# Performance work log

Measured on AMD Instinct MI355X. Metric: run time of the kernel, lower is better.

## Reference

```python
import jax, jax.numpy as jnp
import numpy as np

NUM_EMBEDDINGS = 512
EMBEDDING_DIM = 64
BETA = 0.25


def setup_inputs() -> dict:
    key = jax.random.key(0)
    k1, k2 = jax.random.split(key)
    latent_z = jax.random.normal(k1, (32, EMBEDDING_DIM, 64, 64), dtype=jnp.float32)
    # nn.Embedding init: uniform(-1/K, 1/K)
    scale = 1.0 / NUM_EMBEDDINGS
    embedding = jax.random.uniform(k2, (NUM_EMBEDDINGS, EMBEDDING_DIM), dtype=jnp.float32,
                                   minval=-scale, maxval=scale)
    return {"latent_z": latent_z, "embedding": embedding}


def reference(latent_z, embedding):
    # [B, C, H, W] -> [B, H, W, C]
    z = jnp.transpose(latent_z, (0, 2, 3, 1))
    B, H, W, D = z.shape
    flat_z = z.reshape(-1, D)  # [N, D]

    # squared L2 distances via expansion: ||z||^2 + ||e||^2 - 2 z.e
    dist = (jnp.sum(flat_z ** 2, axis=1, keepdims=True)
            + jnp.sum(embedding ** 2, axis=1)
            - 2.0 * flat_z @ embedding.T)  # [N, K]

    idx = jnp.argmin(dist, axis=1)  # [N]
    encodings = jax.nn.one_hot(idx, NUM_EMBEDDINGS, dtype=flat_z.dtype)  # [N, K]

    # gather codes (same math as one_hot @ embedding)
    quantized = embedding[idx].reshape(B, H, W, D)

    quant_loss = (jnp.mean((jax.lax.stop_gradient(quantized) - z) ** 2)
                  + BETA * jnp.mean((quantized - jax.lax.stop_gradient(z)) ** 2))

    # straight-through estimator
    quantized_st = z + jax.lax.stop_gradient(quantized - z)

    mean_enc = jnp.mean(encodings, axis=0)
    perplexity = jnp.exp(-jnp.sum(mean_enc * jnp.log(mean_enc + 1e-10)))

    quantized_out = jnp.transpose(quantized_st, (0, 3, 1, 2))  # back to [B, C, H, W]
    return quant_loss, quantized_out, perplexity, encodings, idx[:, None]
```

## Files before the change

### kernel.cpp

```cpp
#include <hip/hip_runtime.h>
#include <math.h>

#define NPIX   131072
#define KCODES 512
#define DIM    64
#define HW     4096
#define CHW    262144

#define O_Q    1ll
#define O_PERP 8388609ll
#define O_ENC  8388610ll
#define O_IDX  75497474ll


__device__ __forceinline__ float np_sumsq64(const float (&x)[64]) {
#pragma clang fp contract(off)
  float r0 = x[0]*x[0], r1 = x[1]*x[1], r2 = x[2]*x[2], r3 = x[3]*x[3];
  float r4 = x[4]*x[4], r5 = x[5]*x[5], r6 = x[6]*x[6], r7 = x[7]*x[7];
#pragma unroll
  for (int i = 8; i < 64; i += 8) {
    r0 += x[i+0]*x[i+0];
    r1 += x[i+1]*x[i+1];
    r2 += x[i+2]*x[i+2];
    r3 += x[i+3]*x[i+3];
    r4 += x[i+4]*x[i+4];
    r5 += x[i+5]*x[i+5];
    r6 += x[i+6]*x[i+6];
    r7 += x[i+7]*x[i+7];
  }
  return ((r0+r1)+(r2+r3))+((r4+r5)+(r6+r7));
}

__global__ void vq_prep(const float* __restrict__ emb, float* __restrict__ ws) {
  const int t = threadIdx.x;
  if (t == 0) ws[0] = 0.0f;
  ((unsigned*)ws)[1 + t] = 0u;
  float x[64];
  const float* e = emb + t * DIM;
#pragma unroll
  for (int d = 0; d < 64; ++d) x[d] = e[d];
  ws[513 + t] = np_sumsq64(x);
}

__global__ __launch_bounds__(512, 4)
void vq_main(
    const float* __restrict__ z, const float* __restrict__ emb,
    float* __restrict__ out, float* __restrict__ ws)
{
  __shared__ float ET_s[16 * 256];
  __shared__ float z_l[64 * 128];
  __shared__ float esq_l[512];
  __shared__ float zsq_l[128];
  __shared__ int   ridx_l[128];
  __shared__ float wsum[8];

  const int t   = threadIdx.x;
  const int ci  = t & 31;
  const int pi  = t >> 5;
  const int blk = blockIdx.x;
  const int n0  = blk * 128;
  const int b   = n0 >> 12;
  const int hw0 = n0 & 4095;
  const float* zg = z + (size_t)b * CHW + hw0;

  esq_l[t] = ws[513 + t];

  {
    const int i     = t & 31;
    const int dbase = t >> 5;
#pragma unroll
    for (int r = 0; r < 4; ++r) {
      const int d = dbase + 16 * r;
      *(float4*)&z_l[d * 128 + 4 * i] = *(const float4*)(zg + (size_t)d * HW + 4 * i);
    }
  }

  const int ec = t & 255;
  const int eh = t >> 8;
  float4 p0, p1;
  {
    const float* er = emb + (size_t)ec * 64 + 8 * eh;
    p0 = *(const float4*)(er + 0);
    p1 = *(const float4*)(er + 4);
  }

  __syncthreads();

  if (t < 128) {
    float x[64];
#pragma unroll
    for (int d = 0; d < 64; ++d) x[d] = z_l[d * 128 + t];
    zsq_l[t] = np_sumsq64(x);
  }

  float bd[8];
  int   bk[8];
#pragma unroll
  for (int j = 0; j < 8; ++j) { bd[j] = INFINITY; bk[j] = 0; }

  float2* encb = (float2*)(out + O_ENC) + (size_t)n0 * 256;
  const float2 zz = make_float2(0.0f, 0.0f);

  for (int H = 0; H < 2; ++H) {
    float acc[8][8];
#pragma unroll
    for (int j = 0; j < 8; ++j)
#pragma unroll
      for (int c = 0; c < 8; ++c) acc[j][c] = 0.0f;

    for (int s = 0; s < 4; ++s) {
      __syncthreads();
      {
        const float tmp[8] = {p0.x, p0.y, p0.z, p0.w, p1.x, p1.y, p1.z, p1.w};
#pragma unroll
        for (int dl = 0; dl < 8; ++dl) ET_s[(8 * eh + dl) * 256 + ec] = tmp[dl];
      }
      __syncthreads();

      if (!(H == 1 && s == 3)) {
        const int nH = (s < 3) ? H : 1;
        const int ns = (s < 3) ? (s + 1) : 0;
        const float* er = emb + (size_t)(256 * nH + ec) * 64 + 16 * ns + 8 * eh;
        p0 = *(const float4*)(er + 0);
        p1 = *(const float4*)(er + 4);
      }

      {
        const int batch = 4 * H + s;
#pragma unroll
        for (int u = 0; u < 8; ++u)
          encb[(size_t)batch * 4096 + u * 512 + t] = zz;
      }

#pragma unroll 2
      for (int dl = 0; dl < 16; ++dl) {
        const float* zp = &z_l[(16 * s + dl) * 128 + 8 * pi];
        const float4 za0 = *(const float4*)(zp + 0);
        const float4 za1 = *(const float4*)(zp + 4);
        const float* ep = &ET_s[dl * 256 + 4 * ci];
        const float4 e0 = *(const float4*)(ep + 0);
        const float4 e1 = *(const float4*)(ep + 128);
        const float zr[8] = {za0.x, za0.y, za0.z, za0.w,
                             za1.x, za1.y, za1.z, za1.w};
        const float er_[8] = {e0.x, e0.y, e0.z, e0.w,
                              e1.x, e1.y, e1.z, e1.w};
#pragma unroll
        for (int j = 0; j < 8; ++j)
#pragma unroll
          for (int c = 0; c < 8; ++c)
            acc[j][c] = fmaf(zr[j], er_[c], acc[j][c]);
      }
    }

#pragma unroll
    for (int q = 0; q < 2; ++q)
#pragma unroll
      for (int r = 0; r < 4; ++r) {
        const int k = 256 * H + 128 * q + 4 * ci + r;
        const float eq = esq_l[k];
#pragma unroll
        for (int j = 0; j < 8; ++j) {
          const float dist = (zsq_l[8 * pi + j] + eq) - 2.0f * acc[j][4 * q + r];
          if (dist < bd[j]) { bd[j] = dist; bk[j] = k; }
        }
      }
  }

#pragma unroll
  for (int m = 16; m >= 1; m >>= 1) {
#pragma unroll
    for (int j = 0; j < 8; ++j) {
      const float od = __shfl_xor(bd[j], m, 64);
      const int   ok = __shfl_xor(bk[j], m, 64);
      if (od < bd[j] || (od == bd[j] && ok < bk[j])) { bd[j] = od; bk[j] = ok; }
    }
  }
  if (ci == 0) {
#pragma unroll
    for (int j = 0; j < 8; ++j) ridx_l[8 * pi + j] = bk[j];
  }
  __syncthreads();

  if (t < 128) {
    const int k = ridx_l[t];
    out[O_IDX + n0 + t] = (float)k;
    atomicAdd((unsigned*)ws + 1 + k, 1u);
    out[O_ENC + (size_t)(n0 + t) * 512 + k] = 1.0f;
  }

  {
    const int px = t & 127;
    const int dq = t >> 7;
    const int k  = ridx_l[px];
    const float* e0 = emb + ((size_t)k << 6);
    float* q0 = out + O_Q + (size_t)b * CHW + hw0 + px;
    float lsum = 0.0f;
#pragma unroll
    for (int j = 0; j < 16; ++j) {
      const int d = dq * 16 + j;
      const float ev = e0[d];
      const float df = ev - z_l[d * 128 + px];
      lsum = fmaf(df, df, lsum);
      q0[(size_t)d * HW] = ev;
    }
#pragma unroll
    for (int off = 32; off > 0; off >>= 1) lsum += __shfl_down(lsum, off, 64);
    if ((t & 63) == 0) wsum[t >> 6] = lsum;
  }
  __syncthreads();
  if (t == 0)
    atomicAdd(ws, ((wsum[0] + wsum[1]) + (wsum[2] + wsum[3])) +
                  ((wsum[4] + wsum[5]) + (wsum[6] + wsum[7])));
}

__global__ void vq_fin(float* __restrict__ out, const float* __restrict__ ws) {
  __shared__ float red[8];
  const int t = threadIdx.x;
  const unsigned* counts = (const unsigned*)ws + 1;
  const float p = (float)counts[t] * (1.0f / 131072.0f);
  float h = p * logf(p + 1e-10f);
#pragma unroll
  for (int off = 32; off > 0; off >>= 1) h += __shfl_down(h, off, 64);
  if ((t & 63) == 0) red[t >> 6] = h;
  __syncthreads();
  if (t == 0) {
    float H = 0.0f;
#pragma unroll
    for (int w = 0; w < 8; ++w) H += red[w];
    out[O_PERP] = expf(-H);
    out[0] = 1.25f * ws[0] * (1.0f / 8388608.0f);
  }
}

extern "C" void kernel_launch(void* const* d_in, const int* in_sizes, int n_in,
                              void* d_out, int out_size, void* d_ws, size_t ws_size,
                              hipStream_t stream) {
  const float* z   = (const float*)d_in[0];
  const float* emb = (const float*)d_in[1];
  float* out = (float*)d_out;
  float* ws  = (float*)d_ws;

  vq_prep<<<1, 512, 0, stream>>>(emb, ws);
  vq_main<<<1024, 512, 0, stream>>>(z, emb, out, ws);
  vq_fin<<<1, 512, 0, stream>>>(out, ws);
}
```

Before: 426.0 us.

## Double-buffer codebook tiles and fold finalize into main kernel via last-block reduction

Codebook chunks now go into two alternating shared-memory buffers. This halves the block barriers per chunk and lets the next chunk's transpose-write overlap the current chunk's FMA loop. The separate finalize kernel is removed: the last block to finish, found with an atomic counter, computes perplexity and loss, which saves one kernel launch. In exchange the kernel uses more shared memory, which may reduce occupancy, and adds a threadfence plus an atomic at the end of every block.

```diff
diff --git a/kernel.cpp b/kernel.cpp
--- a/kernel.cpp
+++ b/kernel.cpp
@@ -6,6 +6,7 @@
 #define DIM    64
 #define HW     4096
 #define CHW    262144
+#define NBLK   1024
 
 #define O_Q    1ll
 #define O_PERP 8388609ll
@@ -33,13 +34,81 @@
 
 __global__ void vq_prep(const float* __restrict__ emb, float* __restrict__ ws) {
   const int t = threadIdx.x;
-  if (t == 0) ws[0] = 0.0f;
+  if (t == 0) { ws[0] = 0.0f; ((unsigned*)ws)[1025] = 0u; }
   ((unsigned*)ws)[1 + t] = 0u;
   float x[64];
   const float* e = emb + t * DIM;
 #pragma unroll
   for (int d = 0; d < 64; ++d) x[d] = e[d];
   ws[513 + t] = np_sumsq64(x);
+}
+
+
+__device__ __forceinline__ void et_prefetch(const float* __restrict__ emb,
+                                            int g, int ec, int eh,
+                                            float4& p0, float4& p1) {
+  const float* er = emb + (size_t)(256 * (g >> 2) + ec) * 64
+                        + 16 * (g & 3) + 8 * eh;
+  p0 = *(const float4*)(er + 0);
+  p1 = *(const float4*)(er + 4);
+}
+
+__device__ __forceinline__ void et_write(float* __restrict__ ETb,
+                                         const float4& p0, const float4& p1,
+                                         int eh, int ec) {
+  const float tmp[8] = {p0.x, p0.y, p0.z, p0.w, p1.x, p1.y, p1.z, p1.w};
+#pragma unroll
+  for (int dl = 0; dl < 8; ++dl) ETb[(8 * eh + dl) * 256 + ec] = tmp[dl];
+}
+
+__device__ __forceinline__ void enc_zero(float2* __restrict__ encb, int g, int t) {
+  const float2 zz = make_float2(0.0f, 0.0f);
+#pragma unroll
+  for (int u = 0; u < 8; ++u)
+    encb[(size_t)g * 4096 + u * 512 + t] = zz;
+}
+
+__device__ __forceinline__ void dl_loop(const float* __restrict__ ETb,
+                                        const float* __restrict__ zl,
+                                        int sdim, int pi, int ci,
+                                        float (&acc)[8][8]) {
+#pragma unroll 2
+  for (int dl = 0; dl < 16; ++dl) {
+    const float* zp = &zl[(sdim + dl) * 128 + 8 * pi];
+    const float4 za0 = *(const float4*)(zp + 0);
+    const float4 za1 = *(const float4*)(zp + 4);
+    const float* ep = &ETb[dl * 256 + 4 * ci];
+    const float4 e0 = *(const float4*)(ep + 0);
+    const float4 e1 = *(const float4*)(ep + 128);
+    const float zr[8] = {za0.x, za0.y, za0.z, za0.w,
+                         za1.x, za1.y, za1.z, za1.w};
+    const float er_[8] = {e0.x, e0.y, e0.z, e0.w,
+                          e1.x, e1.y, e1.z, e1.w};
+#pragma unroll
+    for (int j = 0; j < 8; ++j)
+#pragma unroll
+      for (int c = 0; c < 8; ++c)
+        acc[j][c] = fmaf(zr[j], er_[c], acc[j][c]);
+  }
+}
+
+__device__ __forceinline__ void dist_phase(int Hh, int ci, int pi,
+                                           const float (&acc)[8][8],
+                                           const float* __restrict__ esq_l,
+                                           const float* __restrict__ zsq_l,
+                                           float (&bd)[8], int (&bk)[8]) {
+#pragma unroll
+  for (int q = 0; q < 2; ++q)
+#pragma unroll
+    for (int r = 0; r < 4; ++r) {
+      const int k = 256 * Hh + 128 * q + 4 * ci + r;
+      const float eq = esq_l[k];
+#pragma unroll
+      for (int j = 0; j < 8; ++j) {
+        const float dist = (zsq_l[8 * pi + j] + eq) - 2.0f * acc[j][4 * q + r];
+        if (dist < bd[j]) { bd[j] = dist; bk[j] = k; }
+      }
+    }
 }
 
 __global__ __launch_bounds__(512, 4)
@@ -47,12 +116,13 @@
     const float* __restrict__ z, const float* __restrict__ emb,
     float* __restrict__ out, float* __restrict__ ws)
 {
-  __shared__ float ET_s[16 * 256];
+  __shared__ float ET_s[2][16 * 256];
   __shared__ float z_l[64 * 128];
   __shared__ float esq_l[512];
   __shared__ float zsq_l[128];
   __shared__ int   ridx_l[128];
   __shared__ float wsum[8];
+  __shared__ unsigned lflag;
 
   const int t   = threadIdx.x;
   const int ci  = t & 31;
@@ -78,11 +148,7 @@
   const int ec = t & 255;
   const int eh = t >> 8;
   float4 p0, p1;
-  {
-    const float* er = emb + (size_t)ec * 64 + 8 * eh;
-    p0 = *(const float4*)(er + 0);
-    p1 = *(const float4*)(er + 4);
-  }
+  et_prefetch(emb, 0, ec, eh, p0, p1);
 
   __syncthreads();
 
@@ -93,77 +159,51 @@
     zsq_l[t] = np_sumsq64(x);
   }
 
+  et_write(&ET_s[0][0], p0, p1, eh, ec);
+  et_prefetch(emb, 1, ec, eh, p0, p1);
+
+  __syncthreads();
+
   float bd[8];
   int   bk[8];
 #pragma unroll
   for (int j = 0; j < 8; ++j) { bd[j] = INFINITY; bk[j] = 0; }
+  float acc[8][8];
+#pragma unroll
+  for (int j = 0; j < 8; ++j)
+#pragma unroll
+    for (int c = 0; c < 8; ++c) acc[j][c] = 0.0f;
 
   float2* encb = (float2*)(out + O_ENC) + (size_t)n0 * 256;
-  const float2 zz = make_float2(0.0f, 0.0f);
-
-  for (int H = 0; H < 2; ++H) {
-    float acc[8][8];
-#pragma unroll
-    for (int j = 0; j < 8; ++j)
-#pragma unroll
-      for (int c = 0; c < 8; ++c) acc[j][c] = 0.0f;
-
-    for (int s = 0; s < 4; ++s) {
+
+  for (int gg = 0; gg < 4; ++gg) {
+    {
+      const int ge = 2 * gg;
+      et_write(&ET_s[1][0], p0, p1, eh, ec);
+      if (ge < 6) et_prefetch(emb, ge + 2, ec, eh, p0, p1);
+      enc_zero(encb, ge, t);
+      dl_loop(&ET_s[0][0], z_l, 16 * (ge & 3), pi, ci, acc);
       __syncthreads();
-      {
-        const float tmp[8] = {p0.x, p0.y, p0.z, p0.w, p1.x, p1.y, p1.z, p1.w};
-#pragma unroll
-        for (int dl = 0; dl < 8; ++dl) ET_s[(8 * eh + dl) * 256 + ec] = tmp[dl];
+    }
+    {
+      const int go = 2 * gg + 1;
+      if (go < 7) {
+        et_write(&ET_s[0][0], p0, p1, eh, ec);
+        et_prefetch(emb, go + 2, ec, eh, p0, p1);
+      }
+      enc_zero(encb, go, t);
+      dl_loop(&ET_s[1][0], z_l, 16 * (go & 3), pi, ci, acc);
+      if (gg & 1) {
+        dist_phase(gg >> 1, ci, pi, acc, esq_l, zsq_l, bd, bk);
+        if (gg == 1) {
+#pragma unroll
+          for (int j = 0; j < 8; ++j)
+#pragma unroll
+            for (int c = 0; c < 8; ++c) acc[j][c] = 0.0f;
+        }
       }
       __syncthreads();
-
-      if (!(H == 1 && s == 3)) {
-        const int nH = (s < 3) ? H : 1;
-        const int ns = (s < 3) ? (s + 1) : 0;
-        const float* er = emb + (size_t)(256 * nH + ec) * 64 + 16 * ns + 8 * eh;
-        p0 = *(const float4*)(er + 0);
-        p1 = *(const float4*)(er + 4);
-      }
-
-      {
-        const int batch = 4 * H + s;
-#pragma unroll
-        for (int u = 0; u < 8; ++u)
-          encb[(size_t)batch * 4096 + u * 512 + t] = zz;
-      }
-
-#pragma unroll 2
-      for (int dl = 0; dl < 16; ++dl) {
-        const float* zp = &z_l[(16 * s + dl) * 128 + 8 * pi];
-        const float4 za0 = *(const float4*)(zp + 0);
-        const float4 za1 = *(const float4*)(zp + 4);
-        const float* ep = &ET_s[dl * 256 + 4 * ci];
-        const float4 e0 = *(const float4*)(ep + 0);
-        const float4 e1 = *(const float4*)(ep + 128);
-        const float zr[8] = {za0.x, za0.y, za0.z, za0.w,
-                             za1.x, za1.y, za1.z, za1.w};
-        const float er_[8] = {e0.x, e0.y, e0.z, e0.w,
-                              e1.x, e1.y, e1.z, e1.w};
-#pragma unroll
-        for (int j = 0; j < 8; ++j)
-#pragma unroll
-          for (int c = 0; c < 8; ++c)
-            acc[j][c] = fmaf(zr[j], er_[c], acc[j][c]);
-      }
-    }
-
-#pragma unroll
-    for (int q = 0; q < 2; ++q)
-#pragma unroll
-      for (int r = 0; r < 4; ++r) {
-        const int k = 256 * H + 128 * q + 4 * ci + r;
-        const float eq = esq_l[k];
-#pragma unroll
-        for (int j = 0; j < 8; ++j) {
-          const float dist = (zsq_l[8 * pi + j] + eq) - 2.0f * acc[j][4 * q + r];
-          if (dist < bd[j]) { bd[j] = dist; bk[j] = k; }
-        }
-      }
+    }
   }
 
 #pragma unroll
@@ -211,24 +251,29 @@
   if (t == 0)
     atomicAdd(ws, ((wsum[0] + wsum[1]) + (wsum[2] + wsum[3])) +
                   ((wsum[4] + wsum[5]) + (wsum[6] + wsum[7])));
-}
-
-__global__ void vq_fin(float* __restrict__ out, const float* __restrict__ ws) {
-  __shared__ float red[8];
-  const int t = threadIdx.x;
-  const unsigned* counts = (const unsigned*)ws + 1;
-  const float p = (float)counts[t] * (1.0f / 131072.0f);
-  float h = p * logf(p + 1e-10f);
-#pragma unroll
-  for (int off = 32; off > 0; off >>= 1) h += __shfl_down(h, off, 64);
-  if ((t & 63) == 0) red[t >> 6] = h;
+
+  __threadfence();
   __syncthreads();
   if (t == 0) {
-    float H = 0.0f;
-#pragma unroll
-    for (int w = 0; w < 8; ++w) H += red[w];
-    out[O_PERP] = expf(-H);
-    out[0] = 1.25f * ws[0] * (1.0f / 8388608.0f);
+    const unsigned old = atomicAdd((unsigned*)ws + 1025, 1u);
+    lflag = (old == (unsigned)(NBLK - 1)) ? 1u : 0u;
+  }
+  __syncthreads();
+  if (lflag) {
+    const float p = (float)atomicAdd((unsigned*)ws + 1 + t, 0u)
+                    * (1.0f / 131072.0f);
+    float h = p * logf(p + 1e-10f);
+#pragma unroll
+    for (int off = 32; off > 0; off >>= 1) h += __shfl_down(h, off, 64);
+    if ((t & 63) == 0) wsum[t >> 6] = h;
+    __syncthreads();
+    if (t == 0) {
+      float Hs = 0.0f;
+#pragma unroll
+      for (int w = 0; w < 8; ++w) Hs += wsum[w];
+      out[O_PERP] = expf(-Hs);
+      out[0] = 1.25f * atomicAdd(ws, 0.0f) * (1.0f / 8388608.0f);
+    }
   }
 }
 
@@ -241,6 +286,5 @@
   float* ws  = (float*)d_ws;
 
   vq_prep<<<1, 512, 0, stream>>>(emb, ws);
-  vq_main<<<1024, 512, 0, stream>>>(z, emb, out, ws);
-  vq_fin<<<1, 512, 0, stream>>>(out, ws);
-}
+  vq_main<<<NBLK, 512, 0, stream>>>(z, emb, out, ws);
+}
```

After: 744.6 us. 74.8% more time.

## Retile VQ kernel to 64 pixels per block with all 512 codes at once

Applied to the files above, without the earlier changes.

Each block now handles 64 pixels against all 512 codes in one pass. The codebook is staged through a double-buffered transposed LDS tile with two codes interleaved per thread, and z is read directly from global memory (cache) instead of an LDS tile. The grid doubles to 2048 blocks, the one-hot zeroing and quantized writes use nontemporal 8-byte stores, and the z norm is computed as a cross-wave partial sum. This removes one sync per stage and halves the z footprint per block, at the cost of re-reading each codebook tile in twice as many blocks and loading z from global memory in the inner loop.

```diff
diff --git a/kernel.cpp b/kernel.cpp
--- a/kernel.cpp
+++ b/kernel.cpp
@@ -6,6 +6,7 @@
 #define DIM    64
 #define HW     4096
 #define CHW    262144
+#define NBLK   2048
 
 #define O_Q    1ll
 #define O_PERP 8388609ll
@@ -47,127 +48,130 @@
     const float* __restrict__ z, const float* __restrict__ emb,
     float* __restrict__ out, float* __restrict__ ws)
 {
-  __shared__ float ET_s[16 * 256];
-  __shared__ float z_l[64 * 128];
+  __shared__ float ET_s[2][16 * 512];
   __shared__ float esq_l[512];
-  __shared__ float zsq_l[128];
-  __shared__ int   ridx_l[128];
+  __shared__ float zsqp[512];
+  __shared__ float zsq_l[64];
+  __shared__ int   ridx_l[64];
   __shared__ float wsum[8];
 
-  const int t   = threadIdx.x;
-  const int ci  = t & 31;
-  const int pi  = t >> 5;
-  const int blk = blockIdx.x;
-  const int n0  = blk * 128;
-  const int b   = n0 >> 12;
-  const int hw0 = n0 & 4095;
+  const int t    = threadIdx.x;
+  const int lane = t & 63;
+  const int wv   = t >> 6;
+  const int blk  = blockIdx.x;
+  const int n0   = blk * 64;
+  const int b    = n0 >> 12;
+  const int hw0  = n0 & 4095;
   const float* zg = z + (size_t)b * CHW + hw0;
 
   esq_l[t] = ws[513 + t];
 
   {
-    const int i     = t & 31;
-    const int dbase = t >> 5;
-#pragma unroll
-    for (int r = 0; r < 4; ++r) {
-      const int d = dbase + 16 * r;
-      *(float4*)&z_l[d * 128 + 4 * i] = *(const float4*)(zg + (size_t)d * HW + 4 * i);
-    }
-  }
-
-  const int ec = t & 255;
-  const int eh = t >> 8;
-  float4 p0, p1;
-  {
-    const float* er = emb + (size_t)ec * 64 + 8 * eh;
-    p0 = *(const float4*)(er + 0);
-    p1 = *(const float4*)(er + 4);
-  }
-
-  __syncthreads();
-
-  if (t < 128) {
-    float x[64];
-#pragma unroll
-    for (int d = 0; d < 64; ++d) x[d] = z_l[d * 128 + t];
-    zsq_l[t] = np_sumsq64(x);
-  }
+#pragma clang fp contract(off)
+    float r = 0.0f;
+#pragma unroll
+    for (int m = 0; m < 8; ++m) {
+      const float x = zg[(size_t)(8 * m + wv) * HW + lane];
+      r += x * x;
+    }
+    zsqp[t] = r;
+  }
+
+  const int tc = t & 255;
+  const int th = t >> 8;
+  float pa[8], pb[8];
+  {
+    const float* ea = emb + (size_t)(2 * tc) * 64 + 8 * th;
+    const float* eb = ea + 64;
+#pragma unroll
+    for (int i = 0; i < 8; ++i) { pa[i] = ea[i]; pb[i] = eb[i]; }
+  }
+  {
+#pragma unroll
+    for (int i = 0; i < 8; ++i)
+      *(float2*)&ET_s[0][(8 * th + i) * 512 + 2 * tc] = make_float2(pa[i], pb[i]);
+  }
+  {
+    const float* ea = emb + (size_t)(2 * tc) * 64 + 16 + 8 * th;
+    const float* eb = ea + 64;
+#pragma unroll
+    for (int i = 0; i < 8; ++i) { pa[i] = ea[i]; pb[i] = eb[i]; }
+  }
+
+  __syncthreads();
 
   float bd[8];
   int   bk[8];
 #pragma unroll
   for (int j = 0; j < 8; ++j) { bd[j] = INFINITY; bk[j] = 0; }
-
-  float2* encb = (float2*)(out + O_ENC) + (size_t)n0 * 256;
-  const float2 zz = make_float2(0.0f, 0.0f);
-
-  for (int H = 0; H < 2; ++H) {
-    float acc[8][8];
-#pragma unroll
-    for (int j = 0; j < 8; ++j)
-#pragma unroll
-      for (int c = 0; c < 8; ++c) acc[j][c] = 0.0f;
-
-    for (int s = 0; s < 4; ++s) {
-      __syncthreads();
-      {
-        const float tmp[8] = {p0.x, p0.y, p0.z, p0.w, p1.x, p1.y, p1.z, p1.w};
-#pragma unroll
-        for (int dl = 0; dl < 8; ++dl) ET_s[(8 * eh + dl) * 256 + ec] = tmp[dl];
+  float acc[8][8];
+#pragma unroll
+  for (int j = 0; j < 8; ++j)
+#pragma unroll
+    for (int c = 0; c < 8; ++c) acc[j][c] = 0.0f;
+
+  double* encd = (double*)(out + O_ENC) + (size_t)n0 * 256;
+
+  for (int g = 0; g < 4; ++g) {
+    if (g < 3) {
+#pragma unroll
+      for (int i = 0; i < 8; ++i)
+        *(float2*)&ET_s[(g + 1) & 1][(8 * th + i) * 512 + 2 * tc] =
+            make_float2(pa[i], pb[i]);
+    }
+    if (g < 2) {
+      const float* ea = emb + (size_t)(2 * tc) * 64 + 16 * (g + 2) + 8 * th;
+      const float* eb = ea + 64;
+#pragma unroll
+      for (int i = 0; i < 8; ++i) { pa[i] = ea[i]; pb[i] = eb[i]; }
+    }
+#pragma unroll
+    for (int u = 0; u < 8; ++u)
+      __builtin_nontemporal_store(0.0, encd + (size_t)g * 4096 + u * 512 + t);
+    if (g == 0 && t < 64) {
+      zsq_l[t] = ((zsqp[t] + zsqp[64 + t]) + (zsqp[128 + t] + zsqp[192 + t])) +
+                 ((zsqp[256 + t] + zsqp[320 + t]) + (zsqp[384 + t] + zsqp[448 + t]));
+    }
+
+    const float* ETb = &ET_s[g & 1][0];
+#pragma unroll 2
+    for (int dl = 0; dl < 16; ++dl) {
+      const float* zrow = zg + (size_t)(16 * g + dl) * HW + 8 * wv;
+      const float4 za0 = *(const float4*)(zrow + 0);
+      const float4 za1 = *(const float4*)(zrow + 4);
+      const float* ep = &ETb[dl * 512 + 8 * lane];
+      const float4 e0 = *(const float4*)(ep + 0);
+      const float4 e1 = *(const float4*)(ep + 4);
+      const float zr[8] = {za0.x, za0.y, za0.z, za0.w,
+                           za1.x, za1.y, za1.z, za1.w};
+      const float er[8] = {e0.x, e0.y, e0.z, e0.w,
+                           e1.x, e1.y, e1.z, e1.w};
+#pragma unroll
+      for (int j = 0; j < 8; ++j)
+#pragma unroll
+        for (int c = 0; c < 8; ++c)
+          acc[j][c] = fmaf(zr[j], er[c], acc[j][c]);
+    }
+    __syncthreads();
+  }
+
+  {
+    const float4 q0 = *(const float4*)&esq_l[8 * lane];
+    const float4 q1 = *(const float4*)&esq_l[8 * lane + 4];
+    const float eqs[8] = {q0.x, q0.y, q0.z, q0.w, q1.x, q1.y, q1.z, q1.w};
+#pragma unroll
+    for (int r = 0; r < 8; ++r) {
+      const int k = 8 * lane + r;
+#pragma unroll
+      for (int j = 0; j < 8; ++j) {
+        const float dist = (zsq_l[8 * wv + j] + eqs[r]) - 2.0f * acc[j][r];
+        if (dist < bd[j]) { bd[j] = dist; bk[j] = k; }
       }
-      __syncthreads();
-
-      if (!(H == 1 && s == 3)) {
-        const int nH = (s < 3) ? H : 1;
-        const int ns = (s < 3) ? (s + 1) : 0;
-        const float* er = emb + (size_t)(256 * nH + ec) * 64 + 16 * ns + 8 * eh;
-        p0 = *(const float4*)(er + 0);
-        p1 = *(const float4*)(er + 4);
-      }
-
-      {
-        const int batch = 4 * H + s;
-#pragma unroll
-        for (int u = 0; u < 8; ++u)
-          encb[(size_t)batch * 4096 + u * 512 + t] = zz;
-      }
-
-#pragma unroll 2
-      for (int dl = 0; dl < 16; ++dl) {
-        const float* zp = &z_l[(16 * s + dl) * 128 + 8 * pi];
-        const float4 za0 = *(const float4*)(zp + 0);
-        const float4 za1 = *(const float4*)(zp + 4);
-        const float* ep = &ET_s[dl * 256 + 4 * ci];
-        const float4 e0 = *(const float4*)(ep + 0);
-        const float4 e1 = *(const float4*)(ep + 128);
-        const float zr[8] = {za0.x, za0.y, za0.z, za0.w,
-                             za1.x, za1.y, za1.z, za1.w};
-        const float er_[8] = {e0.x, e0.y, e0.z, e0.w,
-                              e1.x, e1.y, e1.z, e1.w};
-#pragma unroll
-        for (int j = 0; j < 8; ++j)
-#pragma unroll
-          for (int c = 0; c < 8; ++c)
-            acc[j][c] = fmaf(zr[j], er_[c], acc[j][c]);
-      }
-    }
-
-#pragma unroll
-    for (int q = 0; q < 2; ++q)
-#pragma unroll
-      for (int r = 0; r < 4; ++r) {
-        const int k = 256 * H + 128 * q + 4 * ci + r;
-        const float eq = esq_l[k];
-#pragma unroll
-        for (int j = 0; j < 8; ++j) {
-          const float dist = (zsq_l[8 * pi + j] + eq) - 2.0f * acc[j][4 * q + r];
-          if (dist < bd[j]) { bd[j] = dist; bk[j] = k; }
-        }
-      }
-  }
-
-#pragma unroll
-  for (int m = 16; m >= 1; m >>= 1) {
+    }
+  }
+
+#pragma unroll
+  for (int m = 32; m >= 1; m >>= 1) {
 #pragma unroll
     for (int j = 0; j < 8; ++j) {
       const float od = __shfl_xor(bd[j], m, 64);
@@ -175,13 +179,13 @@
       if (od < bd[j] || (od == bd[j] && ok < bk[j])) { bd[j] = od; bk[j] = ok; }
     }
   }
-  if (ci == 0) {
-#pragma unroll
-    for (int j = 0; j < 8; ++j) ridx_l[8 * pi + j] = bk[j];
-  }
-  __syncthreads();
-
-  if (t < 128) {
+  if (lane == 0) {
+#pragma unroll
+    for (int j = 0; j < 8; ++j) ridx_l[8 * wv + j] = bk[j];
+  }
+  __syncthreads();
+
+  if (t < 64) {
     const int k = ridx_l[t];
     out[O_IDX + n0 + t] = (float)k;
     atomicAdd((unsigned*)ws + 1 + k, 1u);
@@ -189,23 +193,22 @@
   }
 
   {
-    const int px = t & 127;
-    const int dq = t >> 7;
+    const int px = lane;
     const int k  = ridx_l[px];
     const float* e0 = emb + ((size_t)k << 6);
     float* q0 = out + O_Q + (size_t)b * CHW + hw0 + px;
     float lsum = 0.0f;
 #pragma unroll
-    for (int j = 0; j < 16; ++j) {
-      const int d = dq * 16 + j;
+    for (int j = 0; j < 8; ++j) {
+      const int d = 8 * wv + j;
       const float ev = e0[d];
-      const float df = ev - z_l[d * 128 + px];
+      const float df = ev - zg[(size_t)d * HW + px];
       lsum = fmaf(df, df, lsum);
-      q0[(size_t)d * HW] = ev;
+      __builtin_nontemporal_store(ev, q0 + (size_t)d * HW);
     }
 #pragma unroll
     for (int off = 32; off > 0; off >>= 1) lsum += __shfl_down(lsum, off, 64);
-    if ((t & 63) == 0) wsum[t >> 6] = lsum;
+    if (lane == 0) wsum[wv] = lsum;
   }
   __syncthreads();
   if (t == 0)
@@ -241,6 +244,6 @@
   float* ws  = (float*)d_ws;
 
   vq_prep<<<1, 512, 0, stream>>>(emb, ws);
-  vq_main<<<1024, 512, 0, stream>>>(z, emb, out, ws);
+  vq_main<<<NBLK, 512, 0, stream>>>(z, emb, out, ws);
   vq_fin<<<1, 512, 0, stream>>>(out, ws);
 }
```

New measurement: 480.4 us. 1.13x slower.
